# Kernel optimization log

Hardware: AMD Instinct MI355X
Metric: run time of the kernel (lower is better)

Reference implementation:

```python
import jax, jax.numpy as jnp
import numpy as np

# config: nsql-350M-like, 8 layers
L, D, H, HD, FF, V, RD, MP = 8, 1024, 16, 64, 4096, 51200, 32, 4


def setup_inputs() -> dict:
    key = jax.random.key(0)
    ks = jax.random.split(key, 8)
    B, S = 1, 1024
    s = 0.02
    return {
        'idx': jax.random.randint(ks[0], (B, S), 0, V),
        'input_pos': jnp.arange(S),
        'emb': jax.random.normal(ks[1], (V, D)) * s,
        'Wqkv': jax.random.normal(ks[2], (L, 3 * D, D)) * s,
        'Wo': jax.random.normal(ks[3], (L, D, D)) * s,
        'ln1_w': jnp.ones((L, D)), 'ln1_b': jnp.zeros((L, D)),
        'fc_in_w': jax.random.normal(ks[4], (L, FF, D)) * s,
        'fc_in_b': jnp.zeros((L, FF)),
        'fc_out_w': jax.random.normal(ks[5], (L, D, FF)) * s,
        'fc_out_b': jnp.zeros((L, D)),
        'lnf_w': jnp.ones((D,)), 'lnf_b': jnp.zeros((D,)),
        'lm_w': jax.random.normal(ks[6], (V, D)) * s,
        'lm_b': jnp.zeros((V,)),
    }


def _layer_norm(x, w, b, eps=1e-5):
    mu = jnp.mean(x, axis=-1, keepdims=True)
    var = jnp.var(x, axis=-1, keepdims=True)
    return (x - mu) * jax.lax.rsqrt(var + eps) * w + b


def _new_gelu(x):
    # transformers NewGELUActivation == tanh-approx gelu
    return jax.nn.gelu(x, approximate=True)


def _sincos(input_pos):
    # create_sinusoidal_positions over rotary_dim, gathered at input_pos
    inv_freq = 1.0 / (10000.0 ** (jnp.arange(0, RD, 2, dtype=jnp.float32) / RD))
    ang = input_pos.astype(jnp.float32)[:, None] * inv_freq          # [S, RD/2]
    # repeat_interleave(..., 2, dim=-1) -> interleaved sin/cos, shape [1,S,1,RD]
    sin = jnp.repeat(jnp.sin(ang), 2, axis=-1)[None, :, None, :]
    cos = jnp.repeat(jnp.cos(ang), 2, axis=-1)[None, :, None, :]
    return sin, cos


def _rotary(x, sin, cos):
    # x: [B,S,H,HD]; GPT-J interleaved rotary on first RD dims
    xr, xp = x[..., :RD], x[..., RD:]
    x1, x2 = xr[..., ::2], xr[..., 1::2]
    rot = jnp.stack((-x2, x1), axis=-1).reshape(xr.shape)  # rotate_every_two
    return jnp.concatenate([xr * cos + rot * sin, xp], axis=-1)


def reference(idx, input_pos, emb, Wqkv, Wo, ln1_w, ln1_b, fc_in_w, fc_in_b,
              fc_out_w, fc_out_b, lnf_w, lnf_b, lm_w, lm_b):
    B, S = idx.shape
    x = emb[idx]                                        # [B,S,D]
    sin, cos = _sincos(input_pos)
    causal = jnp.tril(jnp.ones((S, S), dtype=bool))
    neg = jnp.finfo(x.dtype).min
    ld = D // MP

    def split_heads(t):
        # CodeGen _split_heads with mp_num=4: [B,S,MP,ld] -> [B,S,H,HD]
        return t.reshape(B, S, MP, H // MP, HD).reshape(B, S, H, HD)

    for l in range(L):
        h = _layer_norm(x, ln1_w[l], ln1_b[l])
        qkv = (h @ Wqkv[l].T).reshape(B, S, MP, 3 * ld)
        q, v, k = qkv[..., :ld], qkv[..., ld:2 * ld], qkv[..., 2 * ld:]  # q,v,k order!
        q = _rotary(split_heads(q), sin, cos)
        k = _rotary(split_heads(k), sin, cos)
        vh = split_heads(v)
        q, k, vh = (jnp.transpose(t, (0, 2, 1, 3)) for t in (q, k, vh))  # [B,H,S,HD]
        scores = jnp.einsum('bhqd,bhkd->bhqk', q, k) / jnp.sqrt(jnp.asarray(HD, x.dtype))
        scores = jnp.where(causal, scores, neg)
        att = jax.nn.softmax(scores, axis=-1)
        y = jnp.einsum('bhqk,bhkd->bhqd', att, vh)
        y = jnp.transpose(y, (0, 2, 1, 3)).reshape(B, S, D)
        attn_out = y @ Wo[l].T
        mlp = _new_gelu(h @ fc_in_w[l].T + fc_in_b[l]) @ fc_out_w[l].T + fc_out_b[l]
        x = attn_out + mlp + x                          # parallel block + residual

    x = _layer_norm(x, lnf_w, lnf_b)
    return x @ lm_w.T + lm_b                            # [B,S,V]
```

## Files before the change

kernel.cpp:

```cpp
#include <hip/hip_runtime.h>

#define SQ 1024
#define DIM 1024
#define NH 16
#define HDIM 64
#define FFD 4096
#define NV 51200
#define NL 8
#define LDBUF 5120
#define WELEMS ((long)(3 * DIM + DIM + FFD + FFD) * DIM)

typedef __bf16 bf16x8 __attribute__((ext_vector_type(8)));
typedef float f32x4 __attribute__((ext_vector_type(4)));

__device__ __forceinline__ unsigned short f2bf(float f) {
    union { float f; unsigned int i; } v; v.f = f;
    unsigned int r = v.i + 0x7fffu + ((v.i >> 16) & 1u);
    return (unsigned short)(r >> 16);
}
__device__ __forceinline__ float gelu_tanh(float x) {
    float x3 = x * x * x;
    return 0.5f * x * (1.0f + tanhf(0.79788456080286535588f * (x + 0.044715f * x3)));
}
__device__ __forceinline__ void cvt8(const float* __restrict__ s, unsigned short* __restrict__ d, long i) {
    float4 a = *reinterpret_cast<const float4*>(s + i);
    float4 b = *reinterpret_cast<const float4*>(s + i + 4);
    bf16x8 w;
    w[0] = (__bf16)a.x; w[1] = (__bf16)a.y; w[2] = (__bf16)a.z; w[3] = (__bf16)a.w;
    w[4] = (__bf16)b.x; w[5] = (__bf16)b.y; w[6] = (__bf16)b.z; w[7] = (__bf16)b.w;
    *reinterpret_cast<bf16x8*>(d + i) = w;
}

#define GLD16(gp, lp) __builtin_amdgcn_global_load_lds( \
    (__attribute__((address_space(1))) void*)(gp), \
    (__attribute__((address_space(3))) void*)(lp), 16, 0, 0)
#define VMCNT0 asm volatile("s_waitcnt vmcnt(0)" ::: "memory")

__global__ void cvt4_kernel(const float* __restrict__ w0, const float* __restrict__ w1,
                            const float* __restrict__ w2, const float* __restrict__ w3,
                            unsigned short* __restrict__ dst) {
    const int b = blockIdx.x;
    const float* s; long off; unsigned short* d;
    if (b < 1536)      { s = w0; d = dst;                      off = (long)b * 2048; }
    else if (b < 2048) { s = w1; d = dst + (long)3072 * 1024;  off = (long)(b - 1536) * 2048; }
    else if (b < 4096) { s = w2; d = dst + (long)4096 * 1024;  off = (long)(b - 2048) * 2048; }
    else               { s = w3; d = dst + (long)8192 * 1024;  off = (long)(b - 4096) * 2048; }
    cvt8(s, d, off + threadIdx.x * 8);
}
__global__ void cvt_kernel(const float* __restrict__ src, unsigned short* __restrict__ dst) {
    cvt8(src, dst, ((long)blockIdx.x * 256 + threadIdx.x) * 8);
}

__global__ void sincos_kernel(const int* __restrict__ pos, float2* __restrict__ sc) {
    const int t = blockIdx.x * 256 + threadIdx.x;
    if (t >= SQ * 16) return;
    const int s = t >> 4, i = t & 15;
    const float ang = (float)pos[s] * powf(10000.0f, -(float)i / 16.0f);
    sc[t] = make_float2(sinf(ang), cosf(ang));
}

__global__ void embed_kernel(const int* __restrict__ idx, const float* __restrict__ emb,
                             float* __restrict__ x) {
    const int s = blockIdx.x;
    const int d = threadIdx.x * 4;
    const int row = idx[s];
    *reinterpret_cast<float4*>(x + (long)s * DIM + d) =
        *reinterpret_cast<const float4*>(emb + (long)row * DIM + d);
}

template <bool RED>
__global__ __launch_bounds__(256) void ln_kernel(float* __restrict__ x,
                                                 const float* __restrict__ part,
                                                 const float* __restrict__ w,
                                                 const float* __restrict__ b,
                                                 unsigned short* __restrict__ out) {
    __shared__ float red[8];
    const int s = blockIdx.x, tid = threadIdx.x;
    const long fidx = (long)s * 256 + tid;
    float4 v = reinterpret_cast<const float4*>(x)[fidx];
    if (RED) {
        #pragma unroll
        for (int z = 0; z < 8; z++) {
            float4 p = reinterpret_cast<const float4*>(part + (long)z * SQ * DIM)[fidx];
            v.x += p.x; v.y += p.y; v.z += p.z; v.w += p.w;
        }
        reinterpret_cast<float4*>(x)[fidx] = v;
    }
    float sum = v.x + v.y + v.z + v.w;
    float sq = v.x * v.x + v.y * v.y + v.z * v.z + v.w * v.w;
    #pragma unroll
    for (int off = 32; off; off >>= 1) { sum += __shfl_xor(sum, off); sq += __shfl_xor(sq, off); }
    const int wid = tid >> 6, lane = tid & 63;
    if (lane == 0) { red[wid * 2] = sum; red[wid * 2 + 1] = sq; }
    __syncthreads();
    sum = red[0] + red[2] + red[4] + red[6];
    sq  = red[1] + red[3] + red[5] + red[7];
    const float mu = sum * (1.0f / DIM);
    const float var = sq * (1.0f / DIM) - mu * mu;
    const float rstd = rsqrtf(var + 1e-5f);
    const int d = tid * 4;
    float vv[4] = {v.x, v.y, v.z, v.w};
    ushort4 o;
    unsigned short* op = (unsigned short*)&o;
    #pragma unroll
    for (int j = 0; j < 4; j++)
        op[j] = f2bf((vv[j] - mu) * rstd * w[d + j] + b[d + j]);
    *reinterpret_cast<ushort4*>(out + (long)s * DIM + d) = o;
}

__global__ __launch_bounds__(256) void gemm_qkv_fcin(const unsigned short* __restrict__ A,
                                                     const unsigned short* __restrict__ B1,
                                                     const unsigned short* __restrict__ B2,
                                                     const float* __restrict__ bias,
                                                     unsigned short* __restrict__ ffout,
                                                     const float2* __restrict__ sc,
                                                     unsigned short* __restrict__ qt,
                                                     unsigned short* __restrict__ kt,
                                                     unsigned short* __restrict__ vt) {
    __shared__ __align__(16) unsigned short As[2][128 * 64];
    __shared__ __align__(16) unsigned short Bs[2][128 * 64];
    const int tid = threadIdx.x;
    const int nwg = gridDim.x, qch = nwg >> 3;
    const int sb = (blockIdx.x & 7) * qch + (blockIdx.x >> 3);
    const int mb = sb & 7, nb = sb >> 3;
    const int m0 = mb * 128, n0 = nb * 128;
    const int lane = tid & 63, wid = tid >> 6;
    const int l15 = lane & 15, lhi = lane >> 4;
    const int wr = wid >> 1, wc = wid & 1;
    const int sw = l15 & 7;

    const unsigned short* Bbase = B1;
    int nloc = n0;
    if (nb >= 24) { Bbase = B2; nloc = n0 - 3072; }

    f32x4 acc[4][4];
    #pragma unroll
    for (int i = 0; i < 4; i++)
        #pragma unroll
        for (int j = 0; j < 4; j++) acc[i][j] = (f32x4){0.f, 0.f, 0.f, 0.f};

    const int wbase = (tid & ~63) * 8;

    auto stage = [&](int buf, int kt_) {
        const int k0 = kt_ << 6;
        #pragma unroll
        for (int i = 0; i < 4; i++) {
            const int e = (i * 256 + tid) * 8;
            const int r = e >> 6;
            const int cs = (((e >> 3) & 7) ^ (r & 7)) * 8;
            GLD16(A + (long)(m0 + r) * DIM + k0 + cs, &As[buf][i * 2048 + wbase]);
        }
        #pragma unroll
        for (int i = 0; i < 4; i++) {
            const int e = (i * 256 + tid) * 8;
            const int r = e >> 6;
            const int cs = (((e >> 3) & 7) ^ (r & 7)) * 8;
            GLD16(Bbase + (long)(nloc + r) * 1024 + k0 + cs, &Bs[buf][i * 2048 + wbase]);
        }
    };
    auto compute = [&](int buf) {
        #pragma unroll
        for (int ks = 0; ks < 2; ks++) {
            bf16x8 af[4], bfr[4];
            #pragma unroll
            for (int mf = 0; mf < 4; mf++)
                af[mf] = *reinterpret_cast<const bf16x8*>(
                    &As[buf][(wr * 64 + mf * 16 + l15) * 64 + ((ks * 4 + lhi) ^ sw) * 8]);
            #pragma unroll
            for (int nf = 0; nf < 4; nf++)
                bfr[nf] = *reinterpret_cast<const bf16x8*>(
                    &Bs[buf][(wc * 64 + nf * 16 + l15) * 64 + ((ks * 4 + lhi) ^ sw) * 8]);
            #pragma unroll
            for (int mf = 0; mf < 4; mf++)
                #pragma unroll
                for (int nf = 0; nf < 4; nf++)
                    acc[mf][nf] = __builtin_amdgcn_mfma_f32_16x16x32_bf16(af[mf], bfr[nf], acc[mf][nf], 0, 0, 0);
        }
    };

    int cur = 0;
    stage(0, 0);
    VMCNT0; __syncthreads();
    for (int kt_ = 0; kt_ < 16; kt_++) {
        if (kt_ + 1 < 16) stage(cur ^ 1, kt_ + 1);
        compute(cur);
        if (kt_ + 1 < 16) { VMCNT0; __syncthreads(); cur ^= 1; }
    }

    if (nb < 24) {
        #pragma unroll
        for (int nf = 0; nf < 4; nf++) {
            const int col = n0 + wc * 64 + nf * 16 + l15;
            const int g = col / 768;
            const int r768 = col - g * 768;
            const int sec = r768 >> 8;
            const int off = r768 & 255;
            const int h = g * 4 + (off >> 6);
            const int d = off & 63;
            const bool isrot = (d < 32);
            const int dodd = d & 1;
            #pragma unroll
            for (int mf = 0; mf < 4; mf++) {
                #pragma unroll
                for (int j = 0; j < 4; j++) {
                    const int row = m0 + wr * 64 + mf * 16 + lhi * 4 + j;
                    float v = acc[mf][nf][j];
                    const float pv = __shfl_xor(v, 1);
                    float outv = v;
                    if (isrot && sec != 1) {
                        const float2 scv = sc[row * 16 + (d >> 1)];
                        outv = dodd ? (v * scv.y + pv * scv.x)
                                    : (v * scv.y - pv * scv.x);
                    }
                    if (sec == 0)      qt[((long)(h * SQ + row)) * HDIM + d] = f2bf(outv);
                    else if (sec == 2) kt[((long)(h * SQ + row)) * HDIM + d] = f2bf(outv);
                    else               vt[(long)h * (HDIM * SQ) + (long)d * SQ + row] = f2bf(outv);
                }
            }
        }
    } else {
        #pragma unroll
        for (int nf = 0; nf < 4; nf++) {
            const int col = n0 + wc * 64 + nf * 16 + l15;
            #pragma unroll
            for (int mf = 0; mf < 4; mf++) {
                #pragma unroll
                for (int j = 0; j < 4; j++) {
                    const int row = m0 + wr * 64 + mf * 16 + lhi * 4 + j;
                    float v = gelu_tanh(acc[mf][nf][j] + bias[col - 3072]);
                    ffout[(long)row * LDBUF + (col - 3072)] = f2bf(v);
                }
            }
        }
    }
}

__global__ __launch_bounds__(256) void attn_fcout(const unsigned short* __restrict__ qt,
                                                  const unsigned short* __restrict__ kt,
                                                  const unsigned short* __restrict__ vt,
                                                  unsigned short* __restrict__ buf,
                                                  const unsigned short* __restrict__ fcw,
                                                  const float* __restrict__ fcb,
                                                  float* __restrict__ parts,
                                                  const float* __restrict__ nw0,
                                                  const float* __restrict__ nw1,
                                                  const float* __restrict__ nw2,
                                                  const float* __restrict__ nw3,
                                                  unsigned short* __restrict__ nd,
                                                  const float* __restrict__ lmsrc,
                                                  unsigned short* __restrict__ lmdst) {
    __shared__ __align__(16) unsigned short smem[32768];
    const int tid = threadIdx.x, lane = tid & 63, wid = tid >> 6;
    const int l15 = lane & 15, lhi = lane >> 4;
    const int sw = l15 & 7;
    const int wbase = (tid & ~63) * 8;

    if (blockIdx.x < 256) {
        unsigned short* Ks0 = smem;
        unsigned short* Vs0 = smem + 8192;
        unsigned short* Psw = smem + 16384 + wid * 1024;
        const int h = blockIdx.x & 15;
        const int qb = 15 - ((int)blockIdx.x >> 4);
        const int q0 = qb * 64 + wid * 16;

        bf16x8 aq[2];
        {
            const unsigned short* qp = qt + ((long)(h * SQ + q0 + l15)) * HDIM;
            aq[0] = *reinterpret_cast<const bf16x8*>(qp + lhi * 8);
            aq[1] = *reinterpret_cast<const bf16x8*>(qp + 32 + lhi * 8);
        }
        f32x4 o[4];
        #pragma unroll
        for (int nf = 0; nf < 4; nf++) o[nf] = (f32x4){0.f, 0.f, 0.f, 0.f};
        float mrow[4] = {-1e30f, -1e30f, -1e30f, -1e30f};
        float lrow[4] = {0.f, 0.f, 0.f, 0.f};

        auto stageKV = [&](int b, int kv0) {
            #pragma unroll
            for (int i = 0; i < 2; i++) {
                const int e = (i * 256 + tid) * 8;
                const int r = e >> 6;
                const int cs = (((e >> 3) & 7) ^ (r & 7)) * 8;
                GLD16(kt + ((long)(h * SQ + kv0 + r)) * HDIM + cs, Ks0 + b * 4096 + i * 2048 + wbase);
                GLD16(vt + (long)h * (HDIM * SQ) + (long)r * SQ + kv0 + cs, Vs0 + b * 4096 + i * 2048 + wbase);
            }
        };

        int cur = 0;
        stageKV(0, 0);
        VMCNT0; __syncthreads();
        for (int kvt = 0; kvt <= qb; kvt++) {
            const int kv0 = kvt * 64;
            if (kvt < qb) stageKV(cur ^ 1, kv0 + 64);

            f32x4 sa[4];
            #pragma unroll
            for (int hc = 0; hc < 4; hc++) sa[hc] = (f32x4){0.f, 0.f, 0.f, 0.f};
            #pragma unroll
            for (int hc = 0; hc < 4; hc++)
                #pragma unroll
                for (int ks = 0; ks < 2; ks++) {
                    bf16x8 bk = *reinterpret_cast<const bf16x8*>(
                        Ks0 + cur * 4096 + (hc * 16 + l15) * 64 + ((ks * 4 + lhi) ^ sw) * 8);
                    sa[hc] = __builtin_amdgcn_mfma_f32_16x16x32_bf16(aq[ks], bk, sa[hc], 0, 0, 0);
                }
            float pr[4][4], mb[4];
            #pragma unroll
            for (int j = 0; j < 4; j++) {
                const int qi = q0 + lhi * 4 + j;
                #pragma unroll
                for (int hc = 0; hc < 4; hc++) {
                    const int ki = kv0 + hc * 16 + l15;
                    const float sv = sa[hc][j] * 0.125f;
                    pr[hc][j] = (ki <= qi) ? sv : -1e30f;
                }
                mb[j] = fmaxf(fmaxf(pr[0][j], pr[1][j]), fmaxf(pr[2][j], pr[3][j]));
            }
            #pragma unroll
            for (int off = 1; off < 16; off <<= 1)
                #pragma unroll
                for (int j = 0; j < 4; j++) mb[j] = fmaxf(mb[j], __shfl_xor(mb[j], off));
            float alpha[4], psum[4];
            #pragma unroll
            for (int j = 0; j < 4; j++) {
                const float mn = fmaxf(mrow[j], mb[j]);
                alpha[j] = __expf(mrow[j] - mn);
                mrow[j] = mn;
                psum[j] = 0.f;
                #pragma unroll
                for (int hc = 0; hc < 4; hc++) { pr[hc][j] = __expf(pr[hc][j] - mn); psum[j] += pr[hc][j]; }
            }
            #pragma unroll
            for (int off = 1; off < 16; off <<= 1)
                #pragma unroll
                for (int j = 0; j < 4; j++) psum[j] += __shfl_xor(psum[j], off);
            #pragma unroll
            for (int j = 0; j < 4; j++) lrow[j] = lrow[j] * alpha[j] + psum[j];
            #pragma unroll
            for (int nf = 0; nf < 4; nf++)
                #pragma unroll
                for (int j = 0; j < 4; j++) o[nf][j] *= alpha[j];
            #pragma unroll
            for (int hc = 0; hc < 4; hc++)
                #pragma unroll
                for (int j = 0; j < 4; j++) {
                    const int prow = lhi * 4 + j;
                    const int pc8 = (hc * 2 + (l15 >> 3)) ^ (prow & 7);
                    Psw[prow * 64 + pc8 * 8 + (l15 & 7)] = f2bf(pr[hc][j]);
                }
            bf16x8 ap[2];
            ap[0] = *reinterpret_cast<const bf16x8*>(Psw + l15 * 64 + ((0 + lhi) ^ sw) * 8);
            ap[1] = *reinterpret_cast<const bf16x8*>(Psw + l15 * 64 + ((4 + lhi) ^ sw) * 8);
            #pragma unroll
            for (int nf = 0; nf < 4; nf++)
                #pragma unroll
                for (int ks2 = 0; ks2 < 2; ks2++) {
                    bf16x8 bv = *reinterpret_cast<const bf16x8*>(
                        Vs0 + cur * 4096 + (nf * 16 + l15) * 64 + ((ks2 * 4 + lhi) ^ sw) * 8);
                    o[nf] = __builtin_amdgcn_mfma_f32_16x16x32_bf16(ap[ks2], bv, o[nf], 0, 0, 0);
                }
            if (kvt < qb) { VMCNT0; __syncthreads(); cur ^= 1; }
        }
        #pragma unroll
        for (int nf = 0; nf < 4; nf++)
            #pragma unroll
            for (int j = 0; j < 4; j++) {
                const int row = q0 + lhi * 4 + j;
                buf[(long)row * LDBUF + h * HDIM + nf * 16 + l15] = f2bf(o[nf][j] / lrow[j]);
            }
    } else if (blockIdx.x < 768) {
        unsigned short* As0 = smem;
        unsigned short* Bs0 = smem + 16384;
        const int b2 = (int)blockIdx.x - 256;
        const int sb = (b2 & 7) * 64 + (b2 >> 3);
        const int kz = sb & 7, nb = (sb >> 3) & 7, mb = sb >> 6;
        const int m0 = mb * 128, n0 = nb * 128;
        const int kt0 = kz * 8;
        const int wr = wid >> 1, wc = wid & 1;
        const unsigned short* Aff = buf + DIM;

        f32x4 acc[4][4];
        #pragma unroll
        for (int i = 0; i < 4; i++)
            #pragma unroll
            for (int j = 0; j < 4; j++) acc[i][j] = (f32x4){0.f, 0.f, 0.f, 0.f};

        auto stage = [&](int bf_, int kt_) {
            const int k0 = kt_ << 6;
            #pragma unroll
            for (int i = 0; i < 4; i++) {
                const int e = (i * 256 + tid) * 8;
                const int r = e >> 6;
                const int cs = (((e >> 3) & 7) ^ (r & 7)) * 8;
                GLD16(Aff + (long)(m0 + r) * LDBUF + k0 + cs, As0 + bf_ * 8192 + i * 2048 + wbase);
                GLD16(fcw + (long)(n0 + r) * FFD + k0 + cs, Bs0 + bf_ * 8192 + i * 2048 + wbase);
            }
        };
        auto compute = [&](int bf_) {
            #pragma unroll
            for (int ks = 0; ks < 2; ks++) {
                bf16x8 af[4], bfr[4];
                #pragma unroll
                for (int mf = 0; mf < 4; mf++)
                    af[mf] = *reinterpret_cast<const bf16x8*>(
                        As0 + bf_ * 8192 + (wr * 64 + mf * 16 + l15) * 64 + ((ks * 4 + lhi) ^ sw) * 8);
                #pragma unroll
                for (int nf = 0; nf < 4; nf++)
                    bfr[nf] = *reinterpret_cast<const bf16x8*>(
                        Bs0 + bf_ * 8192 + (wc * 64 + nf * 16 + l15) * 64 + ((ks * 4 + lhi) ^ sw) * 8);
                #pragma unroll
                for (int mf = 0; mf < 4; mf++)
                    #pragma unroll
                    for (int nf = 0; nf < 4; nf++)
                        acc[mf][nf] = __builtin_amdgcn_mfma_f32_16x16x32_bf16(af[mf], bfr[nf], acc[mf][nf], 0, 0, 0);
            }
        };

        int cur = 0;
        stage(0, kt0);
        VMCNT0; __syncthreads();
        for (int t = 0; t < 8; t++) {
            if (t + 1 < 8) stage(cur ^ 1, kt0 + t + 1);
            compute(cur);
            if (t + 1 < 8) { VMCNT0; __syncthreads(); cur ^= 1; }
        }

        float* P = parts + (long)kz * SQ * DIM;
        #pragma unroll
        for (int nf = 0; nf < 4; nf++) {
            const int col = n0 + wc * 64 + nf * 16 + l15;
            const float bv = (kz == 0) ? fcb[col] : 0.f;
            #pragma unroll
            for (int mf = 0; mf < 4; mf++) {
                #pragma unroll
                for (int j = 0; j < 4; j++) {
                    const int row = m0 + wr * 64 + mf * 16 + lhi * 4 + j;
                    P[(long)row * DIM + col] = acc[mf][nf][j] + bv;
                }
            }
        }
    } else {
        const int cb = (int)blockIdx.x - 768;
        const int nch = (int)gridDim.x - 768;
        const long stride = (long)nch * 256;
        const long base = (long)cb * 256 + tid;
        if (nd) {
            const long n0v = (long)3072 * 1024 / 8, n1v = (long)1024 * 1024 / 8;
            const long n2v = (long)4096 * 1024 / 8, n3v = (long)4096 * 1024 / 8;
            for (long i = base; i < n0v; i += stride) cvt8(nw0, nd, i * 8);
            unsigned short* d1 = nd + n0v * 8;
            for (long i = base; i < n1v; i += stride) cvt8(nw1, d1, i * 8);
            unsigned short* d2 = d1 + n1v * 8;
            for (long i = base; i < n2v; i += stride) cvt8(nw2, d2, i * 8);
            unsigned short* d3 = d2 + n2v * 8;
            for (long i = base; i < n3v; i += stride) cvt8(nw3, d3, i * 8);
        }
        if (lmdst) {
            const long nlmv = (long)(NV / NL) * DIM / 8;
            for (long i = base; i < nlmv; i += stride) cvt8(lmsrc, lmdst, i * 8);
        }
    }
}

__global__ __launch_bounds__(256) void wo_rmw(const unsigned short* __restrict__ buf,
                                              const unsigned short* __restrict__ wo,
                                              float* __restrict__ parts) {
    __shared__ __align__(16) unsigned short As[2][128 * 64];
    __shared__ __align__(16) unsigned short Bs[2][128 * 64];
    const int tid = threadIdx.x;
    const int sb = (blockIdx.x & 7) * 32 + (blockIdx.x >> 3);
    const int kz = sb & 3, nb = (sb >> 2) & 7, mb = sb >> 5;
    const int m0 = mb * 128, n0 = nb * 128;
    const int kt0 = kz * 4;
    const int lane = tid & 63, wid = tid >> 6;
    const int l15 = lane & 15, lhi = lane >> 4;
    const int wr = wid >> 1, wc = wid & 1;
    const int sw = l15 & 7;
    const int wbase = (tid & ~63) * 8;

    f32x4 acc[4][4];
    #pragma unroll
    for (int i = 0; i < 4; i++)
        #pragma unroll
        for (int j = 0; j < 4; j++) acc[i][j] = (f32x4){0.f, 0.f, 0.f, 0.f};

    auto stage = [&](int bf_, int kt_) {
        const int k0 = kt_ << 6;
        #pragma unroll
        for (int i = 0; i < 4; i++) {
            const int e = (i * 256 + tid) * 8;
            const int r = e >> 6;
            const int cs = (((e >> 3) & 7) ^ (r & 7)) * 8;
            GLD16(buf + (long)(m0 + r) * LDBUF + k0 + cs, &As[bf_][i * 2048 + wbase]);
            GLD16(wo + (long)(n0 + r) * DIM + k0 + cs, &Bs[bf_][i * 2048 + wbase]);
        }
    };
    auto compute = [&](int bf_) {
        #pragma unroll
        for (int ks = 0; ks < 2; ks++) {
            bf16x8 af[4], bfr[4];
            #pragma unroll
            for (int mf = 0; mf < 4; mf++)
                af[mf] = *reinterpret_cast<const bf16x8*>(
                    &As[bf_][(wr * 64 + mf * 16 + l15) * 64 + ((ks * 4 + lhi) ^ sw) * 8]);
            #pragma unroll
            for (int nf = 0; nf < 4; nf++)
                bfr[nf] = *reinterpret_cast<const bf16x8*>(
                    &Bs[bf_][(wc * 64 + nf * 16 + l15) * 64 + ((ks * 4 + lhi) ^ sw) * 8]);
            #pragma unroll
            for (int mf = 0; mf < 4; mf++)
                #pragma unroll
                for (int nf = 0; nf < 4; nf++)
                    acc[mf][nf] = __builtin_amdgcn_mfma_f32_16x16x32_bf16(af[mf], bfr[nf], acc[mf][nf], 0, 0, 0);
        }
    };

    int cur = 0;
    stage(0, kt0);
    VMCNT0; __syncthreads();
    for (int t = 0; t < 4; t++) {
        if (t + 1 < 4) stage(cur ^ 1, kt0 + t + 1);
        compute(cur);
        if (t + 1 < 4) { VMCNT0; __syncthreads(); cur ^= 1; }
    }

    float* P = parts + (long)kz * SQ * DIM;
    #pragma unroll
    for (int nf = 0; nf < 4; nf++) {
        const int col = n0 + wc * 64 + nf * 16 + l15;
        #pragma unroll
        for (int mf = 0; mf < 4; mf++) {
            #pragma unroll
            for (int j = 0; j < 4; j++) {
                const int row = m0 + wr * 64 + mf * 16 + lhi * 4 + j;
                P[(long)row * DIM + col] += acc[mf][nf][j];
            }
        }
    }
}

__global__ __launch_bounds__(512) void gemm256(const unsigned short* __restrict__ A,
                                               const unsigned short* __restrict__ B,
                                               const float* __restrict__ bias,
                                               float* __restrict__ C) {
    __shared__ __align__(16) unsigned short As[2][256 * 64];
    __shared__ __align__(16) unsigned short Bs[2][256 * 64];
    const int tid = threadIdx.x;
    const int nwg = gridDim.x, qch = nwg >> 3;
    const int sb = (blockIdx.x & 7) * qch + (blockIdx.x >> 3);
    const int mb = sb & 3, nb = sb >> 2;
    const int m0 = mb * 256, n0 = nb * 256;
    const int lane = tid & 63, wid = tid >> 6;
    const int l15 = lane & 15, lhi = lane >> 4;
    const int wm = wid >> 2, wn = wid & 3;
    const int sw = l15 & 7;

    f32x4 acc[8][4];
    #pragma unroll
    for (int i = 0; i < 8; i++)
        #pragma unroll
        for (int j = 0; j < 4; j++) acc[i][j] = (f32x4){0.f, 0.f, 0.f, 0.f};

    const int wbase = (tid & ~63) * 8;

    auto stage = [&](int buf, int kt) {
        const int k0 = kt << 6;
        #pragma unroll
        for (int i = 0; i < 4; i++) {
            const int e = (i * 512 + tid) * 8;
            const int r = e >> 6;
            const int cs = (((e >> 3) & 7) ^ (r & 7)) * 8;
            GLD16(A + (long)(m0 + r) * 1024 + k0 + cs, &As[buf][i * 4096 + wbase]);
            GLD16(B + (long)(n0 + r) * 1024 + k0 + cs, &Bs[buf][i * 4096 + wbase]);
        }
    };
    auto compute = [&](int buf) {
        #pragma unroll
        for (int ks = 0; ks < 2; ks++) {
            bf16x8 af[8], bfr[4];
            #pragma unroll
            for (int mf = 0; mf < 8; mf++)
                af[mf] = *reinterpret_cast<const bf16x8*>(
                    &As[buf][(wm * 128 + mf * 16 + l15) * 64 + ((ks * 4 + lhi) ^ sw) * 8]);
            #pragma unroll
            for (int nf = 0; nf < 4; nf++)
                bfr[nf] = *reinterpret_cast<const bf16x8*>(
                    &Bs[buf][(wn * 64 + nf * 16 + l15) * 64 + ((ks * 4 + lhi) ^ sw) * 8]);
            #pragma unroll
            for (int mf = 0; mf < 8; mf++)
                #pragma unroll
                for (int nf = 0; nf < 4; nf++)
                    acc[mf][nf] = __builtin_amdgcn_mfma_f32_16x16x32_bf16(af[mf], bfr[nf], acc[mf][nf], 0, 0, 0);
        }
    };

    int cur = 0;
    stage(0, 0);
    VMCNT0; __syncthreads();
    for (int kt = 0; kt < 16; kt++) {
        if (kt < 15) stage(cur ^ 1, kt + 1);
        compute(cur);
        if (kt < 15) { VMCNT0; __syncthreads(); cur ^= 1; }
    }

    #pragma unroll
    for (int nf = 0; nf < 4; nf++) {
        const int col = n0 + wn * 64 + nf * 16 + l15;
        const float bv = bias[col];
        #pragma unroll
        for (int mf = 0; mf < 8; mf++) {
            #pragma unroll
            for (int j = 0; j < 4; j++) {
                const int row = m0 + wm * 128 + mf * 16 + lhi * 4 + j;
                C[(long)row * NV + col] = acc[mf][nf][j] + bv;
            }
        }
    }
}

extern "C" void kernel_launch(void* const* d_in, const int* in_sizes, int n_in,
                              void* d_out, int out_size, void* d_ws, size_t ws_size,
                              hipStream_t stream) {
    const int* idx    = (const int*)d_in[0];
    const int* pos    = (const int*)d_in[1];
    const float* emb  = (const float*)d_in[2];
    const float* Wqkv = (const float*)d_in[3];
    const float* Wo   = (const float*)d_in[4];
    const float* ln1w = (const float*)d_in[5];
    const float* ln1b = (const float*)d_in[6];
    const float* fciw = (const float*)d_in[7];
    const float* fcib = (const float*)d_in[8];
    const float* fcow = (const float*)d_in[9];
    const float* fcob = (const float*)d_in[10];
    const float* lnfw = (const float*)d_in[11];
    const float* lnfb = (const float*)d_in[12];
    const float* lmw  = (const float*)d_in[13];
    const float* lmb  = (const float*)d_in[14];

    const long tailBytes = (long)SQ * DIM * 4 + (long)8 * SQ * DIM * 4 + (long)SQ * DIM * 2
                         + (long)3 * NH * SQ * HDIM * 2 + (long)SQ * LDBUF * 2 + (long)SQ * 16 * 8;
    const long bigBytes  = 2 * WELEMS * 2 + (long)NV * DIM * 2 + tailBytes;
    const bool big = (long)ws_size >= bigBytes + (1 << 20);

    char* ws = (char*)d_ws;
    unsigned short *wbufA, *wbufB, *lmbuf;
    if (big) {
        wbufA = (unsigned short*)ws; ws += WELEMS * 2;
        wbufB = (unsigned short*)ws; ws += WELEMS * 2;
        lmbuf = (unsigned short*)ws; ws += (long)NV * DIM * 2;
    } else {
        wbufA = (unsigned short*)ws; ws += (long)NV * DIM * 2;
        wbufB = wbufA;
        lmbuf = wbufA;
    }
    float* x           = (float*)ws;          ws += (long)SQ * DIM * 4;
    float* parts       = (float*)ws;          ws += (long)8 * SQ * DIM * 4;
    unsigned short* h  = (unsigned short*)ws; ws += (long)SQ * DIM * 2;
    unsigned short* qt = (unsigned short*)ws; ws += (long)NH * SQ * HDIM * 2;
    unsigned short* kt = (unsigned short*)ws; ws += (long)NH * SQ * HDIM * 2;
    unsigned short* vt = (unsigned short*)ws; ws += (long)NH * SQ * HDIM * 2;
    unsigned short* buf= (unsigned short*)ws; ws += (long)SQ * LDBUF * 2;
    float2* sc         = (float2*)ws;         ws += (long)SQ * 16 * 8;

    auto wq = [&](unsigned short* wb) { return wb; };
    auto wo_ = [&](unsigned short* wb) { return wb + (long)3072 * 1024; };
    auto wfi = [&](unsigned short* wb) { return wb + (long)4096 * 1024; };
    auto wfo = [&](unsigned short* wb) { return wb + (long)8192 * 1024; };

    sincos_kernel<<<64, 256, 0, stream>>>(pos, sc);
    embed_kernel<<<SQ, 256, 0, stream>>>(idx, emb, x);
    cvt4_kernel<<<6144, 256, 0, stream>>>(Wqkv, Wo, fciw, fcow, wbufA);

    for (int l = 0; l < NL; l++) {
        unsigned short* wb = (l & 1) ? wbufB : wbufA;
        unsigned short* wn = (l & 1) ? wbufA : wbufB;

        if (!big && l > 0)
            cvt4_kernel<<<6144, 256, 0, stream>>>(Wqkv + (long)l * 3 * DIM * DIM,
                                                  Wo   + (long)l * DIM * DIM,
                                                  fciw + (long)l * FFD * DIM,
                                                  fcow + (long)l * DIM * FFD, wb);

        if (l == 0) ln_kernel<false><<<SQ, 256, 0, stream>>>(x, nullptr, ln1w, ln1b, h);
        else ln_kernel<true><<<SQ, 256, 0, stream>>>(x, parts, ln1w + (long)l * DIM, ln1b + (long)l * DIM, h);

        gemm_qkv_fcin<<<448, 256, 0, stream>>>(h, wq(wb), wfi(wb), fcib + (long)l * FFD,
                                               buf + DIM, sc, qt, kt, vt);
        if (big) {
            const int nl = l + 1;
            const float* n0 = (nl < NL) ? Wqkv + (long)nl * 3 * DIM * DIM : nullptr;
            const float* n1 = (nl < NL) ? Wo   + (long)nl * DIM * DIM : nullptr;
            const float* n2 = (nl < NL) ? fciw + (long)nl * FFD * DIM : nullptr;
            const float* n3 = (nl < NL) ? fcow + (long)nl * DIM * FFD : nullptr;
            unsigned short* ndst = (nl < NL) ? wn : nullptr;
            attn_fcout<<<768 + 512, 256, 0, stream>>>(qt, kt, vt, buf, wfo(wb),
                                                      fcob + (long)l * DIM, parts,
                                                      n0, n1, n2, n3, ndst,
                                                      lmw + (long)l * (NV / NL) * DIM,
                                                      lmbuf + (long)l * (NV / NL) * DIM);
        } else {
            attn_fcout<<<768, 256, 0, stream>>>(qt, kt, vt, buf, wfo(wb),
                                                fcob + (long)l * DIM, parts,
                                                nullptr, nullptr, nullptr, nullptr, nullptr,
                                                nullptr, nullptr);
        }
        wo_rmw<<<256, 256, 0, stream>>>(buf, wo_(wb), parts);
    }
    if (!big) cvt_kernel<<<25600, 256, 0, stream>>>(lmw, lmbuf);
    ln_kernel<true><<<SQ, 256, 0, stream>>>(x, parts, lnfw, lnfb, h);
    gemm256<<<800, 512, 0, stream>>>(h, lmbuf, lmb, (float*)d_out);
}
```

Before: 1.030 ms.

## Rebalance split-K, move LM-weight conversion into QKV GEMM, split LM head

The fc_out split-K drops from 8 to 4 partitions with longer K loops, which halves the partial-sum buffers and the reduction reads in layer norm. The LM-head weight conversion now runs in extra blocks of the QKV/fc_in GEMM launch instead of the attention launch, which rebalances the background work between kernels. The final LM head is split into a 256-tile kernel for the first half of the columns and a new 128-tile kernel for the second half, likely to reduce tail imbalance. The cost is fewer split-K blocks (less parallelism in fc_out) and an extra kernel launch.

After: 1.053 ms. 1.02x slower.

```diff
diff --git a/kernel.cpp b/kernel.cpp
--- a/kernel.cpp
+++ b/kernel.cpp
@@ -80,7 +80,7 @@
     float4 v = reinterpret_cast<const float4*>(x)[fidx];
     if (RED) {
         #pragma unroll
-        for (int z = 0; z < 8; z++) {
+        for (int z = 0; z < 4; z++) {
             float4 p = reinterpret_cast<const float4*>(part + (long)z * SQ * DIM)[fidx];
             v.x += p.x; v.y += p.y; v.z += p.z; v.w += p.w;
         }
@@ -116,12 +116,22 @@
                                                      const float2* __restrict__ sc,
                                                      unsigned short* __restrict__ qt,
                                                      unsigned short* __restrict__ kt,
-                                                     unsigned short* __restrict__ vt) {
+                                                     unsigned short* __restrict__ vt,
+                                                     const float* __restrict__ lmsrc,
+                                                     unsigned short* __restrict__ lmdst) {
     __shared__ __align__(16) unsigned short As[2][128 * 64];
     __shared__ __align__(16) unsigned short Bs[2][128 * 64];
     const int tid = threadIdx.x;
-    const int nwg = gridDim.x, qch = nwg >> 3;
-    const int sb = (blockIdx.x & 7) * qch + (blockIdx.x >> 3);
+    if (blockIdx.x >= 448) {
+        if (lmdst) {
+            const int cb = (int)blockIdx.x - 448;
+            const long stride = (long)((int)gridDim.x - 448) * 256;
+            const long nlmv = (long)(NV / NL) * DIM / 8;
+            for (long i = (long)cb * 256 + tid; i < nlmv; i += stride) cvt8(lmsrc, lmdst, i * 8);
+        }
+        return;
+    }
+    const int sb = (blockIdx.x & 7) * 56 + (blockIdx.x >> 3);
     const int mb = sb & 7, nb = sb >> 3;
     const int m0 = mb * 128, n0 = nb * 128;
     const int lane = tid & 63, wid = tid >> 6;
@@ -246,9 +256,7 @@
                                                   const float* __restrict__ nw1,
                                                   const float* __restrict__ nw2,
                                                   const float* __restrict__ nw3,
-                                                  unsigned short* __restrict__ nd,
-                                                  const float* __restrict__ lmsrc,
-                                                  unsigned short* __restrict__ lmdst) {
+                                                  unsigned short* __restrict__ nd) {
     __shared__ __align__(16) unsigned short smem[32768];
     const int tid = threadIdx.x, lane = tid & 63, wid = tid >> 6;
     const int l15 = lane & 15, lhi = lane >> 4;
@@ -368,14 +376,14 @@
                 const int row = q0 + lhi * 4 + j;
                 buf[(long)row * LDBUF + h * HDIM + nf * 16 + l15] = f2bf(o[nf][j] / lrow[j]);
             }
-    } else if (blockIdx.x < 768) {
+    } else if (blockIdx.x < 512) {
         unsigned short* As0 = smem;
         unsigned short* Bs0 = smem + 16384;
         const int b2 = (int)blockIdx.x - 256;
-        const int sb = (b2 & 7) * 64 + (b2 >> 3);
-        const int kz = sb & 7, nb = (sb >> 3) & 7, mb = sb >> 6;
+        const int sb = (b2 & 7) * 32 + (b2 >> 3);
+        const int kz = sb & 3, nb = (sb >> 2) & 7, mb = sb >> 5;
         const int m0 = mb * 128, n0 = nb * 128;
-        const int kt0 = kz * 8;
+        const int kt0 = kz * 16;
         const int wr = wid >> 1, wc = wid & 1;
         const unsigned short* Aff = buf + DIM;
 
@@ -419,10 +427,10 @@
         int cur = 0;
         stage(0, kt0);
         VMCNT0; __syncthreads();
-        for (int t = 0; t < 8; t++) {
-            if (t + 1 < 8) stage(cur ^ 1, kt0 + t + 1);
+        for (int t = 0; t < 16; t++) {
+            if (t + 1 < 16) stage(cur ^ 1, kt0 + t + 1);
             compute(cur);
-            if (t + 1 < 8) { VMCNT0; __syncthreads(); cur ^= 1; }
+            if (t + 1 < 16) { VMCNT0; __syncthreads(); cur ^= 1; }
         }
 
         float* P = parts + (long)kz * SQ * DIM;
@@ -440,11 +448,10 @@
             }
         }
     } else {
-        const int cb = (int)blockIdx.x - 768;
-        const int nch = (int)gridDim.x - 768;
-        const long stride = (long)nch * 256;
-        const long base = (long)cb * 256 + tid;
         if (nd) {
+            const int cb = (int)blockIdx.x - 512;
+            const long stride = (long)((int)gridDim.x - 512) * 256;
+            const long base = (long)cb * 256 + tid;
             const long n0v = (long)3072 * 1024 / 8, n1v = (long)1024 * 1024 / 8;
             const long n2v = (long)4096 * 1024 / 8, n3v = (long)4096 * 1024 / 8;
             for (long i = base; i < n0v; i += stride) cvt8(nw0, nd, i * 8);
@@ -454,10 +461,6 @@
             for (long i = base; i < n2v; i += stride) cvt8(nw2, d2, i * 8);
             unsigned short* d3 = d2 + n2v * 8;
             for (long i = base; i < n3v; i += stride) cvt8(nw3, d3, i * 8);
-        }
-        if (lmdst) {
-            const long nlmv = (long)(NV / NL) * DIM / 8;
-            for (long i = base; i < nlmv; i += stride) cvt8(lmsrc, lmdst, i * 8);
         }
     }
 }
@@ -612,6 +615,84 @@
             #pragma unroll
             for (int j = 0; j < 4; j++) {
                 const int row = m0 + wm * 128 + mf * 16 + lhi * 4 + j;
+                C[(long)row * NV + col] = acc[mf][nf][j] + bv;
+            }
+        }
+    }
+}
+
+__global__ __launch_bounds__(256) void gemm128lm(const unsigned short* __restrict__ A,
+                                                 const unsigned short* __restrict__ B,
+                                                 const float* __restrict__ bias,
+                                                 float* __restrict__ C, int coff) {
+    __shared__ __align__(16) unsigned short As[2][128 * 64];
+    __shared__ __align__(16) unsigned short Bs[2][128 * 64];
+    const int tid = threadIdx.x;
+    const int nwg = gridDim.x, qch = nwg >> 3;
+    const int sb = (blockIdx.x & 7) * qch + (blockIdx.x >> 3);
+    const int mb = sb & 7, nb = sb >> 3;
+    const int m0 = mb * 128, n0 = coff + nb * 128;
+    const int lane = tid & 63, wid = tid >> 6;
+    const int l15 = lane & 15, lhi = lane >> 4;
+    const int wr = wid >> 1, wc = wid & 1;
+    const int sw = l15 & 7;
+    const int wbase = (tid & ~63) * 8;
+
+    f32x4 acc[4][4];
+    #pragma unroll
+    for (int i = 0; i < 4; i++)
+        #pragma unroll
+        for (int j = 0; j < 4; j++) acc[i][j] = (f32x4){0.f, 0.f, 0.f, 0.f};
+
+    auto stage = [&](int buf, int kt_) {
+        const int k0 = kt_ << 6;
+        #pragma unroll
+        for (int i = 0; i < 4; i++) {
+            const int e = (i * 256 + tid) * 8;
+            const int r = e >> 6;
+            const int cs = (((e >> 3) & 7) ^ (r & 7)) * 8;
+            GLD16(A + (long)(m0 + r) * 1024 + k0 + cs, &As[buf][i * 2048 + wbase]);
+            GLD16(B + (long)(n0 + r) * 1024 + k0 + cs, &Bs[buf][i * 2048 + wbase]);
+        }
+    };
+    auto compute = [&](int buf) {
+        #pragma unroll
+        for (int ks = 0; ks < 2; ks++) {
+            bf16x8 af[4], bfr[4];
+            #pragma unroll
+            for (int mf = 0; mf < 4; mf++)
+                af[mf] = *reinterpret_cast<const bf16x8*>(
+                    &As[buf][(wr * 64 + mf * 16 + l15) * 64 + ((ks * 4 + lhi) ^ sw) * 8]);
+            #pragma unroll
+            for (int nf = 0; nf < 4; nf++)
+                bfr[nf] = *reinterpret_cast<const bf16x8*>(
+                    &Bs[buf][(wc * 64 + nf * 16 + l15) * 64 + ((ks * 4 + lhi) ^ sw) * 8]);
+            #pragma unroll
+            for (int mf = 0; mf < 4; mf++)
+                #pragma unroll
+                for (int nf = 0; nf < 4; nf++)
+                    acc[mf][nf] = __builtin_amdgcn_mfma_f32_16x16x32_bf16(af[mf], bfr[nf], acc[mf][nf], 0, 0, 0);
+        }
+    };
+
+    int cur = 0;
+    stage(0, 0);
+    VMCNT0; __syncthreads();
+    for (int kt_ = 0; kt_ < 16; kt_++) {
+        if (kt_ + 1 < 16) stage(cur ^ 1, kt_ + 1);
+        compute(cur);
+        if (kt_ + 1 < 16) { VMCNT0; __syncthreads(); cur ^= 1; }
+    }
+
+    #pragma unroll
+    for (int nf = 0; nf < 4; nf++) {
+        const int col = n0 + wc * 64 + nf * 16 + l15;
+        const float bv = bias[col];
+        #pragma unroll
+        for (int mf = 0; mf < 4; mf++) {
+            #pragma unroll
+            for (int j = 0; j < 4; j++) {
+                const int row = m0 + wr * 64 + mf * 16 + lhi * 4 + j;
                 C[(long)row * NV + col] = acc[mf][nf][j] + bv;
             }
         }
@@ -637,7 +718,7 @@
     const float* lmw  = (const float*)d_in[13];
     const float* lmb  = (const float*)d_in[14];
 
-    const long tailBytes = (long)SQ * DIM * 4 + (long)8 * SQ * DIM * 4 + (long)SQ * DIM * 2
+    const long tailBytes = (long)SQ * DIM * 4 + (long)4 * SQ * DIM * 4 + (long)SQ * DIM * 2
                          + (long)3 * NH * SQ * HDIM * 2 + (long)SQ * LDBUF * 2 + (long)SQ * 16 * 8;
     const long bigBytes  = 2 * WELEMS * 2 + (long)NV * DIM * 2 + tailBytes;
     const bool big = (long)ws_size >= bigBytes + (1 << 20);
@@ -654,7 +735,7 @@
         lmbuf = wbufA;
     }
     float* x           = (float*)ws;          ws += (long)SQ * DIM * 4;
-    float* parts       = (float*)ws;          ws += (long)8 * SQ * DIM * 4;
+    float* parts       = (float*)ws;          ws += (long)4 * SQ * DIM * 4;
     unsigned short* h  = (unsigned short*)ws; ws += (long)SQ * DIM * 2;
     unsigned short* qt = (unsigned short*)ws; ws += (long)NH * SQ * HDIM * 2;
     unsigned short* kt = (unsigned short*)ws; ws += (long)NH * SQ * HDIM * 2;
@@ -684,29 +765,28 @@
         if (l == 0) ln_kernel<false><<<SQ, 256, 0, stream>>>(x, nullptr, ln1w, ln1b, h);
         else ln_kernel<true><<<SQ, 256, 0, stream>>>(x, parts, ln1w + (long)l * DIM, ln1b + (long)l * DIM, h);
 
-        gemm_qkv_fcin<<<448, 256, 0, stream>>>(h, wq(wb), wfi(wb), fcib + (long)l * FFD,
-                                               buf + DIM, sc, qt, kt, vt);
+        gemm_qkv_fcin<<<704, 256, 0, stream>>>(h, wq(wb), wfi(wb), fcib + (long)l * FFD,
+                                               buf + DIM, sc, qt, kt, vt,
+                                               big ? lmw + (long)l * (NV / NL) * DIM : nullptr,
+                                               big ? lmbuf + (long)l * (NV / NL) * DIM : nullptr);
         if (big) {
             const int nl = l + 1;
-            const float* n0 = (nl < NL) ? Wqkv + (long)nl * 3 * DIM * DIM : nullptr;
-            const float* n1 = (nl < NL) ? Wo   + (long)nl * DIM * DIM : nullptr;
-            const float* n2 = (nl < NL) ? fciw + (long)nl * FFD * DIM : nullptr;
-            const float* n3 = (nl < NL) ? fcow + (long)nl * DIM * FFD : nullptr;
-            unsigned short* ndst = (nl < NL) ? wn : nullptr;
-            attn_fcout<<<768 + 512, 256, 0, stream>>>(qt, kt, vt, buf, wfo(wb),
-                                                      fcob + (long)l * DIM, parts,
-                                                      n0, n1, n2, n3, ndst,
-                                                      lmw + (long)l * (NV / NL) * DIM,
-                                                      lmbuf + (long)l * (NV / NL) * DIM);
+            attn_fcout<<<1024, 256, 0, stream>>>(qt, kt, vt, buf, wfo(wb),
+                                                 fcob + (long)l * DIM, parts,
+                                                 (nl < NL) ? Wqkv + (long)nl * 3 * DIM * DIM : nullptr,
+                                                 (nl < NL) ? Wo   + (long)nl * DIM * DIM : nullptr,
+                                                 (nl < NL) ? fciw + (long)nl * FFD * DIM : nullptr,
+                                                 (nl < NL) ? fcow + (long)nl * DIM * FFD : nullptr,
+                                                 (nl < NL) ? wn : nullptr);
         } else {
-            attn_fcout<<<768, 256, 0, stream>>>(qt, kt, vt, buf, wfo(wb),
+            attn_fcout<<<512, 256, 0, stream>>>(qt, kt, vt, buf, wfo(wb),
                                                 fcob + (long)l * DIM, parts,
-                                                nullptr, nullptr, nullptr, nullptr, nullptr,
-                                                nullptr, nullptr);
+                                                nullptr, nullptr, nullptr, nullptr, nullptr);
         }
         wo_rmw<<<256, 256, 0, stream>>>(buf, wo_(wb), parts);
     }
     if (!big) cvt_kernel<<<25600, 256, 0, stream>>>(lmw, lmbuf);
     ln_kernel<true><<<SQ, 256, 0, stream>>>(x, parts, lnfw, lnfb, h);
-    gemm256<<<800, 512, 0, stream>>>(h, lmbuf, lmb, (float*)d_out);
-}
+    gemm256<<<400, 512, 0, stream>>>(h, lmbuf, lmb, (float*)d_out);
+    gemm128lm<<<1600, 256, 0, stream>>>(h, lmbuf, lmb, (float*)d_out, 25600);
+}
```
